# Kernel tuning notes

Measured on AMD Instinct MI355X. Metric: run time of the kernel, lower is better.

## Reference

```python
import jax, jax.numpy as jnp
import numpy as np

# ---- static problem constants ----
B, N, L = 8, 256, 15.0          # molecules, atoms per molecule, cubic cell length (Angstrom)
DL, SIGMA = 1.5, 1.0            # Ewald k-space spacing and Gaussian smearing width
ELEMENTS = np.array([1, 6, 7, 8])
NORM_FACTOR = (1.0 / 90.0474) ** 0.5
TWO_PI = 2.0 * np.pi
KSQ_MAX = (TWO_PI / DL) ** 2
NMAX = int(np.ceil(L / DL))     # 10 -> (2*10+1)^3 = 9261 k-vectors
_g = np.arange(-NMAX, NMAX + 1)
K_GRID = jnp.asarray(np.stack(np.meshgrid(_g, _g, _g, indexing='ij'), -1)
                     .reshape(-1, 3).astype(np.float32))  # [K,3] integer k indices
_zmap = np.full(int(ELEMENTS.max()) + 1, -1)
for _i, _z in enumerate(ELEMENTS):
    _zmap[_z] = _i
Z_INDEX_MAP = jnp.asarray(_zmap)


def setup_inputs() -> dict:
    key = jax.random.key(0)
    k1, k2, k3, k4 = jax.random.split(key, 4)
    positions = jax.random.uniform(k1, (B * N, 3), jnp.float32) * L
    cell = jnp.tile((L * jnp.eye(3, dtype=jnp.float32))[None], (B, 1, 1))
    chi = jax.random.normal(k2, (B * N,), jnp.float32)
    idx = jax.random.randint(k3, (B * N,), 0, len(ELEMENTS))
    atomic_numbers = jnp.asarray(ELEMENTS)[idx]
    batch = jnp.repeat(jnp.arange(B), N)
    J_raw = jax.random.uniform(k4, (len(ELEMENTS),), jnp.float32, 0.5, 1.5)
    system_charge = jnp.zeros((B,), jnp.float32)
    return dict(positions=positions, cell=cell, chi=chi, J_raw=J_raw,
                system_charge=system_charge, atomic_numbers=atomic_numbers, batch=batch)


def _a_matrix(r, cell):
    """Reciprocal-space Ewald interaction matrix A (energy = 0.5 q^T A q), one molecule."""
    recip = TWO_PI * jnp.linalg.inv(cell).T            # rows: reciprocal lattice vectors
    k = K_GRID @ recip                                 # [K,3]
    k2 = jnp.sum(k * k, axis=-1)                       # [K]
    valid = (k2 > 1e-10) & (k2 < KSQ_MAX)
    f = jnp.where(valid, jnp.exp(-0.5 * SIGMA * SIGMA * k2) / jnp.maximum(k2, 1e-10), 0.0)
    vol = jnp.abs(jnp.linalg.det(cell))
    kr = r @ k.T                                       # [N,K]
    c, s = jnp.cos(kr), jnp.sin(kr)
    # A_ij = (4*pi/V) sum_k f(k) cos(k.(r_i - r_j))
    A = (2.0 * TWO_PI / vol) * ((c * f) @ c.T + (s * f) @ s.T)
    # remove Gaussian self-interaction: E_self = -sum_i q_i^2 / (sigma*sqrt(2*pi))
    A = A - (2.0 / (SIGMA * np.sqrt(TWO_PI))) * jnp.eye(N, dtype=r.dtype)
    return A


def _solve_qeq(A, chi_m, J_i, Q):
    """Charge-equilibration with Lagrange multiplier for total-charge constraint."""
    coeffs = jnp.ones((N + 1, N + 1), A.dtype)
    coeffs = coeffs.at[:N, :N].set(A + jnp.diag(J_i))
    coeffs = coeffs.at[N, N].set(0.0)
    rhs = jnp.concatenate([-chi_m, (Q / NORM_FACTOR)[None].astype(A.dtype)])
    sol = jnp.linalg.solve(coeffs, rhs)
    q = sol[:N]
    e = 0.5 * q @ (A @ q)
    return q, e


def reference(positions, cell, chi, J_raw, system_charge, atomic_numbers, batch):
    r = positions.reshape(B, N, 3)
    chi_b = chi.reshape(B, N)
    J_elem = jnp.square(J_raw)
    J_i = J_elem[Z_INDEX_MAP[atomic_numbers]].reshape(B, N)
    A = jax.vmap(_a_matrix)(r, cell)                   # [B,N,N]
    q, e = jax.vmap(_solve_qeq)(A, chi_b, J_i, system_charge)
    all_q_eq = q.reshape(B * N, 1)
    all_ewald = e                                      # [B]
    return all_q_eq, all_ewald
```

## Files before the change

### kernel.cpp

```cpp
#include <hip/hip_runtime.h>
#include <math.h>

#define NBATCH 8
#define NATOM  256
#define NP1    257
#define WROW   258
#define TOTALK 9261
#define KCAP   2560
#define KC     16
#define NB     16
#define UBW    124
#define BDF    768
#define BDB    256
#define FLAGOFF 2528
#define SLOTMAX 2500

#define TWO_PI_D 6.283185307179586
#define DIAG_SUB 0.7978845608028654

__device__ __constant__ int TI10[10] = {0,0,0,0,1,1,1,2,2,3};
__device__ __constant__ int TJ10[10] = {0,1,2,3,1,2,3,2,3,3};

struct GemmSh {
  int4   kn[KC];
  double kw[KC];
  double cI[KC][64], sI[KC][64];
  double cJ[KC][64], sJ[KC][64];
};

__device__ __forceinline__ void atomAddD(double* p, double v) {
#if defined(__has_builtin)
#if __has_builtin(__builtin_amdgcn_global_atomic_fadd_f64)
  __builtin_amdgcn_global_atomic_fadd_f64(p, v);
  return;
#endif
#endif
  unsigned long long* u = (unsigned long long*)p;
  unsigned long long old = *u, assumed;
  do {
    assumed = old;
    old = atomicCAS(u, assumed,
                    (unsigned long long)__double_as_longlong(
                        v + __longlong_as_double((long long)assumed)));
  } while (old != assumed);
}

__device__ __forceinline__ void classify2(const void* c0, const void* c1, const void* c2,
                                          const float*& chi, const int*& znum)
{
  const void* cands[3] = {c0, c1, c2};
  int got = 0;
  for (int i = 0; i < 3; i++) {
    unsigned uu = ((const unsigned*)cands[i])[0];
    if (uu == 0u) continue;
    else if (uu < 16u) { znum = (const int*)cands[i]; got |= 1; }
    else               { chi  = (const float*)cands[i]; got |= 2; }
  }
  if (got != 3) { chi = (const float*)c0; znum = (const int*)c1; }
}

__global__ __launch_bounds__(256) void zero_planes(
    double* __restrict__ P0g, int4* __restrict__ klist, int nplanes)
{
  if (blockIdx.x == 0 && threadIdx.x < 256) {
    const int b = threadIdx.x >> 5, s = threadIdx.x & 31;
    klist[(size_t)b*KCAP + FLAGOFF + s] = make_int4(0, 0, 0, 0);
  }
  const size_t npair = (size_t)nplanes * NBATCH * ((NP1*WROW) >> 1);
  double2* Z = (double2*)P0g;
  const double2 z = make_double2(0.0, 0.0);
  for (size_t i = (size_t)blockIdx.x*256 + threadIdx.x; i < npair;
       i += (size_t)gridDim.x*256)
    Z[i] = z;
}

__global__ __launch_bounds__(256) void prep(
    const float* __restrict__ pos, const float* __restrict__ cell,
    double2* __restrict__ Tg, int4* __restrict__ klist,
    double* __restrict__ kw, int* __restrict__ kcount,
    const void* __restrict__ c0, const void* __restrict__ c1, const void* __restrict__ c2,
    const float* __restrict__ syschg,
    double* __restrict__ P0g, int nplanes)
{
  const int b = blockIdx.x;
  const int tid = threadIdx.x;
  __shared__ double ivs[9];
  __shared__ double prefs;
  __shared__ int cnt;
  if (tid == 0) {
    double c[9];
#pragma unroll
    for (int i = 0; i < 9; i++) c[i] = (double)cell[b*9+i];
    double det = c[0]*(c[4]*c[8]-c[5]*c[7]) - c[1]*(c[3]*c[8]-c[5]*c[6])
               + c[2]*(c[3]*c[7]-c[4]*c[6]);
    double idet = 1.0/det;
    ivs[0]=(c[4]*c[8]-c[5]*c[7])*idet; ivs[1]=(c[2]*c[7]-c[1]*c[8])*idet; ivs[2]=(c[1]*c[5]-c[2]*c[4])*idet;
    ivs[3]=(c[5]*c[6]-c[3]*c[8])*idet; ivs[4]=(c[0]*c[8]-c[2]*c[6])*idet; ivs[5]=(c[2]*c[3]-c[0]*c[5])*idet;
    ivs[6]=(c[3]*c[7]-c[4]*c[6])*idet; ivs[7]=(c[1]*c[6]-c[0]*c[7])*idet; ivs[8]=(c[0]*c[4]-c[1]*c[3])*idet;
    prefs = 2.0*TWO_PI_D/fabs(det);
    cnt = 0;
  }
  __syncthreads();
  {
    const int a = tid;
    double x = (double)pos[((size_t)b*NATOM+a)*3+0];
    double y = (double)pos[((size_t)b*NATOM+a)*3+1];
    double z = (double)pos[((size_t)b*NATOM+a)*3+2];
    double u[3];
    u[0] = TWO_PI_D*(ivs[0]*x + ivs[3]*y + ivs[6]*z);
    u[1] = TWO_PI_D*(ivs[1]*x + ivs[4]*y + ivs[7]*z);
    u[2] = TWO_PI_D*(ivs[2]*x + ivs[5]*y + ivs[8]*z);
#pragma unroll
    for (int d = 0; d < 3; d++) {
      double2* T = Tg + (size_t)((b*3 + d)*21)*256;
      double c1 = cos(u[d]);
      double s1 = sin(u[d]);
      T[10*256 + a] = make_double2(1.0, 0.0);
      T[11*256 + a] = make_double2(c1,  s1);
      T[ 9*256 + a] = make_double2(c1, -s1);
      double cp = c1, sp = s1;
      for (int n = 2; n <= 10; n++) {
        double cn = cp*c1 - sp*s1;
        double sn = sp*c1 + cp*s1;
        cp = cn; sp = sn;
        T[(10+n)*256 + a] = make_double2(cp,  sp);
        T[(10-n)*256 + a] = make_double2(cp, -sp);
      }
    }
  }
  const double ksqmax = (TWO_PI_D/1.5)*(TWO_PI_D/1.5);
  for (int m = tid; m < TOTALK; m += 256) {
    int n1 = m/441 - 10;
    int n2 = (m/21)%21 - 10;
    int n3 = m%21 - 10;
    bool half = (n1 > 0) || (n1 == 0 && (n2 > 0 || (n2 == 0 && n3 > 0)));
    if (!half) continue;
    double d1 = n1, d2 = n2, d3 = n3;
    double kx = TWO_PI_D*(ivs[0]*d1 + ivs[1]*d2 + ivs[2]*d3);
    double ky = TWO_PI_D*(ivs[3]*d1 + ivs[4]*d2 + ivs[5]*d3);
    double kz = TWO_PI_D*(ivs[6]*d1 + ivs[7]*d2 + ivs[8]*d3);
    double k2 = kx*kx + ky*ky + kz*kz;
    if (k2 > 1e-10 && k2 < ksqmax) {
      double w = 2.0 * prefs * exp(-0.5*k2) / k2;
      int slot = atomicAdd(&cnt, 1);
      if (slot < SLOTMAX) {
        klist[b*KCAP + slot] = make_int4(n1, n2, n3, 0);
        kw[b*KCAP + slot] = w;
      }
    }
  }
  __syncthreads();
  {
    const float* chi = nullptr; const int* znum = nullptr;
    classify2(c0, c1, c2, chi, znum);
    double* P0b = P0g + (size_t)b*NP1*WROW;
    for (int i = tid; i < NATOM; i += 256) {
      P0b[(size_t)NATOM*WROW + i] = 1.0;
      P0b[(size_t)i*WROW + NATOM] = 1.0;
      P0b[(size_t)i*WROW + 257]   = -(double)chi[b*NATOM + i];
    }
    if (tid == 0) {
      P0b[(size_t)NATOM*WROW + NATOM] = 0.0;
      P0b[(size_t)NATOM*WROW + 257]   = (double)syschg[b]*sqrt(90.0474);
      kcount[b] = (cnt < SLOTMAX) ? cnt : SLOTMAX;
    }
  }
}

__device__ void gemm_tile(int b, int ti, int tj, int tid,
                          const double2* __restrict__ Tg,
                          const int4* __restrict__ klist,
                          const double* __restrict__ kw, int ks, int ke,
                          double* __restrict__ Ab, bool mirror, GemmSh& S)
{
  const int tx = tid & 15, ty = tid >> 4;
  const int ro = ty << 2, co = tx << 2;
  double acc[16];
#pragma unroll
  for (int i = 0; i < 16; i++) acc[i] = 0.0;

  for (int k0 = ks; k0 < ke; k0 += KC) {
    if (tid < KC) {
      int kk = k0 + tid;
      if (kk < ke) { S.kn[tid] = klist[b*KCAP + kk]; S.kw[tid] = kw[b*KCAP + kk]; }
      else         { S.kn[tid] = make_int4(0,0,0,0); S.kw[tid] = 0.0; }
    }
    __syncthreads();
#pragma unroll
    for (int p = 0; p < 8; p++) {
      int idx = p*256 + tid;
      int a    = idx & 63;
      int kk   = (idx >> 6) & (KC-1);
      int side = idx >> 10;
      int atom = ((side == 0) ? ti : tj) + a;
      int4 nn = S.kn[kk];
      double2 t1 = Tg[(size_t)((b*3+0)*21 + (nn.x+10))*256 + atom];
      double2 t2 = Tg[(size_t)((b*3+1)*21 + (nn.y+10))*256 + atom];
      double2 t3 = Tg[(size_t)((b*3+2)*21 + (nn.z+10))*256 + atom];
      double ex = t1.x*t2.x - t1.y*t2.y;
      double ey = t1.x*t2.y + t1.y*t2.x;
      double cx = ex*t3.x - ey*t3.y;
      double cy = ex*t3.y + ey*t3.x;
      if (side == 0) { double w = S.kw[kk]; S.cI[kk][a] = w*cx; S.sI[kk][a] = w*cy; }
      else           { S.cJ[kk][a] = cx; S.sJ[kk][a] = cy; }
    }
    __syncthreads();
#pragma unroll
    for (int kk = 0; kk < KC; kk++) {
      double ci[4], si[4], cj[4], sj[4];
#pragma unroll
      for (int r = 0; r < 2; r++) {
        double2 v0 = *(const double2*)&S.cI[kk][ro + 2*r];
        ci[2*r] = v0.x; ci[2*r+1] = v0.y;
        double2 v1 = *(const double2*)&S.sI[kk][ro + 2*r];
        si[2*r] = v1.x; si[2*r+1] = v1.y;
        double2 v2 = *(const double2*)&S.cJ[kk][co + 2*r];
        cj[2*r] = v2.x; cj[2*r+1] = v2.y;
        double2 v3 = *(const double2*)&S.sJ[kk][co + 2*r];
        sj[2*r] = v3.x; sj[2*r+1] = v3.y;
      }
#pragma unroll
      for (int r = 0; r < 4; r++)
#pragma unroll
        for (int c = 0; c < 4; c++)
          acc[r*4+c] += ci[r]*cj[c] + si[r]*sj[c];
    }
    __syncthreads();
  }
#pragma unroll
  for (int r = 0; r < 4; r++) {
#pragma unroll
    for (int c = 0; c < 4; c++) {
      int gr = ti + ro + r, gc = tj + co + c;
      double v = acc[r*4+c];
      atomAddD(&Ab[(size_t)gr*WROW + gc], v);
      if (mirror && ti != tj) atomAddD(&Ab[(size_t)gc*WROW + gr], v);
    }
  }
}

__device__ __forceinline__ double* plane_sel(double* P0, double* P1, double* P2, int s) {
  return (s == 0) ? P0 : ((s == 1) ? P1 : P2);
}

__global__ __launch_bounds__(256) void build_A_gemm(
    const double2* __restrict__ Tg, const int4* __restrict__ klist,
    const double* __restrict__ kw, const int* __restrict__ kcount,
    double* __restrict__ P0g, double* __restrict__ P1g, double* __restrict__ P2g,
    int nplanes)
{
  __shared__ GemmSh S;
  const int nseg = 2*nplanes;
  const int u = blockIdx.x;
  const int seg = u / 80;
  const int r = u - seg*80;
  const int b = r / 10;
  const int t = r - b*10;
  const int s = (seg < nplanes) ? seg : (seg - nplanes);
  const int cnt = kcount[b];
  const int ks = (int)((long long)cnt * seg / nseg);
  const int ke = (int)((long long)cnt * (seg+1) / nseg);
  double* Ab = plane_sel(P0g, P1g, P2g, s) + (size_t)b*NP1*WROW;
  gemm_tile(b, TI10[t]*64, TJ10[t]*64, threadIdx.x, Tg, klist, kw, ks, ke, Ab, true, S);
}

__global__ __launch_bounds__(BDF, 2) void solve_factor(
    double* __restrict__ P0g, const double* __restrict__ P1g, const double* __restrict__ P2g,
    int nplanes,
    const void* __restrict__ c0, const void* __restrict__ c1, const void* __restrict__ c2,
    const float* __restrict__ Jraw,
    int4* __restrict__ klist, double* __restrict__ U11g)
{
  const int b = blockIdx.x >> 1;
  const int h = blockIdx.x & 1;
  const int tid = threadIdx.x;
  double* Pb = P0g + (size_t)b*NP1*WROW;
  const double* Qb = P1g + (size_t)b*NP1*WROW;
  const double* Rb = P2g + (size_t)b*NP1*WROW;
  const bool two   = (nplanes > 1);
  const bool three = (nplanes > 2);
  int* FA = (int*)(klist + (size_t)b*KCAP + FLAGOFF);
  int* FB = FA + 32;
  double* U11b = U11g + (size_t)b*17*256;

  __shared__ __align__(16) double pan[NP1+4][NB+2];
  __shared__ double dnv[NB];
  __shared__ __align__(16) double Ub[NB][UBW];

  const float* chi = nullptr; const int* znum = nullptr;
  classify2(c0, c1, c2, chi, znum);
  const float J0 = Jraw[0], J1 = Jraw[1], J2 = Jraw[2], J3 = Jraw[3];

  int p = 0;
  for (int p0 = 0; p0 < NP1; p0 += NB, p++) {
    const int pw  = (NB < NP1 - p0) ? NB : (NP1 - p0);
    const int nr  = NP1 - p0;
    const int nrt = nr - pw;
    const int tc0 = p0 + pw;
    const int tc  = WROW - tc0;
    const bool first = (p0 == 0);
    int leftCols = (tc >= 4) ? (((tc >> 1) + 1) & ~1) : tc;
    const int clo = (h == 0) ? tc0 : tc0 + leftCols;
    const int chiC = (h == 0) ? tc0 + leftCols : tc0 + tc;
    const int ownCols = chiC - clo;
    if (p > 0) {
      if (tid == 0) {
        while (atomicAdd(&FA[p-1], 0) == 0) __builtin_amdgcn_s_sleep(2);
        while (atomicAdd(&FB[p-1], 0) == 0) __builtin_amdgcn_s_sleep(2);
        __threadfence();
      }
      __syncthreads();
    }
    for (int idx = tid; idx < nr*pw; idx += BDF) {
      int r, c;
      if (pw == NB) { r = idx >> 4; c = idx & 15; } else { r = idx; c = 0; }
      double v;
      if (first) {
        size_t a = (size_t)r*WROW + c;
        v = Pb[a];
        if (two)   v += Qb[a];
        if (three) v += Rb[a];
        if (r == c) {
          int z = znum[b*NATOM + r];
          float Jr = (z == 1) ? J0 : (z == 6) ? J1 : (z == 7) ? J2 : J3;
          v += (double)Jr*(double)Jr - DIAG_SUB;
        }
      } else {
        v = Pb[(size_t)(p0+r)*WROW + p0 + c];
      }
      pan[r][c] = v;
    }
    __syncthreads();
    if (pw == NB) {
      if (tid < NB) {
        double v[NB];
#pragma unroll
        for (int c = 0; c < NB; c++) v[c] = pan[tid][c];
#pragma unroll
        for (int c = 0; c < NB; c++) {
          double piv = __shfl(v[c], c);
          double dinv = 1.0 / piv;
          if (tid == c) dnv[c] = dinv;
          double f = v[c] * dinv;
#pragma unroll
          for (int cc = 0; cc < NB; cc++) {
            if (cc > c) {
              double ucc = __shfl(v[cc], c);
              if (tid > c) v[cc] -= f * ucc;
            }
          }
          if (tid > c) v[c] = f;
        }
#pragma unroll
        for (int c = 0; c < NB; c++) pan[tid][c] = v[c];
      }
    }
    __syncthreads();
    if (pw == NB) {
      if (tid < nrt) {
        const int r = NB + tid;
        double w[NB];
#pragma unroll
        for (int c = 0; c < NB; c++) w[c] = pan[r][c];
#pragma unroll
        for (int c = 0; c < NB; c++) {
          double s = w[c];
#pragma unroll
          for (int c2 = 0; c2 < NB; c2++) if (c2 < c) s -= w[c2] * pan[c2][c];
          w[c] = s * dnv[c];
        }
#pragma unroll
        for (int c = 0; c < NB; c++) pan[r][c] = w[c];
      } else if (tid >= 256 && tid < 256 + ownCols) {
        const int j = clo + (tid - 256);
        double v[NB];
#pragma unroll
        for (int c = 0; c < NB; c++) {
          size_t a = (size_t)(p0+c)*WROW + j;
          double t = Pb[a];
          if (first) {
            if (two)   t += Qb[a];
            if (three) t += Rb[a];
          }
          v[c] = t;
        }
#pragma unroll
        for (int c = 0; c < NB; c++)
#pragma unroll
          for (int r2 = 0; r2 < NB; r2++) if (r2 > c) v[r2] -= pan[r2][c]*v[c];
#pragma unroll
        for (int c = 0; c < NB; c++) {
          Pb[(size_t)(p0+c)*WROW + j] = v[c];
          Ub[c][tid - 256] = v[c];
        }
      } else if (h == 0 && tid >= 512) {
        const int idx = tid - 512;
        U11b[p*256 + idx] = pan[idx >> 4][idx & 15];
      }
    } else {
      if (h == 0 && tid == 0) U11b[16*256] = pan[0][0];
    }
    __syncthreads();
    if (pw == NB && ownCols > 0 && nrt > 0) {
      const int jp   = tid & 63;
      const int rowg = tid >> 6;
      if (clo + 2*jp < chiC) {
        const int jrel = (clo - tc0) + 2*jp;
        double va[NB], vb[NB];
#pragma unroll
        for (int c = 0; c < NB; c++) {
          double2 u = *(const double2*)&Ub[c][2*jp];
          va[c] = u.x; vb[c] = u.y;
        }
        auto loadrow = [&](int rr, double2& x0, double2& x1) {
          x0 = make_double2(0.0, 0.0); x1 = x0;
          if (rr < nrt) {
            const int row0 = tc0 + rr;
            const size_t ad = (size_t)row0*WROW + tc0 + jrel;
            x0 = *(const double2*)&Pb[ad];
            if (rr + 1 < nrt) x1 = *(const double2*)&Pb[ad + WROW];
            if (first) {
              if (two) {
                double2 q0 = *(const double2*)&Qb[ad]; x0.x += q0.x; x0.y += q0.y;
                if (rr + 1 < nrt) { double2 q1 = *(const double2*)&Qb[ad + WROW]; x1.x += q1.x; x1.y += q1.y; }
              }
              if (three) {
                double2 r0v = *(const double2*)&Rb[ad]; x0.x += r0v.x; x0.y += r0v.y;
                if (rr + 1 < nrt) { double2 r1v = *(const double2*)&Rb[ad + WROW]; x1.x += r1v.x; x1.y += r1v.y; }
              }
              if (rr == jrel) {
                const int row0g = tc0 + rr;
                if (row0g < NATOM) {
                  int z = znum[b*NATOM + row0g];
                  float Jr = (z == 1) ? J0 : (z == 6) ? J1 : (z == 7) ? J2 : J3;
                  x0.x += (double)Jr*(double)Jr - DIAG_SUB;
                }
                if (rr + 1 < nrt && row0g + 1 < NATOM) {
                  int z = znum[b*NATOM + row0g + 1];
                  float Jr = (z == 1) ? J0 : (z == 6) ? J1 : (z == 7) ? J2 : J3;
                  x1.y += (double)Jr*(double)Jr - DIAG_SUB;
                }
              }
            }
          }
        };
        int rr = 2*rowg;
        double2 a0, a1;
        loadrow(rr, a0, a1);
        while (rr < nrt) {
          const int rn = rr + 24;
          double2 n0, n1;
          loadrow(rn, n0, n1);
          const double* pr0 = pan[NB + rr];
          const double* pr1 = pan[NB + rr + 1];
#pragma unroll
          for (int m = 0; m < NB/2; m++) {
            double2 l0 = *(const double2*)&pr0[2*m];
            double2 l1 = *(const double2*)&pr1[2*m];
            a0.x -= l0.x*va[2*m] + l0.y*va[2*m+1];
            a0.y -= l0.x*vb[2*m] + l0.y*vb[2*m+1];
            a1.x -= l1.x*va[2*m] + l1.y*va[2*m+1];
            a1.y -= l1.x*vb[2*m] + l1.y*vb[2*m+1];
          }
          const size_t ad = (size_t)(tc0+rr)*WROW + tc0 + jrel;
          *(double2*)&Pb[ad] = a0;
          if (rr + 1 < nrt) *(double2*)&Pb[ad + WROW] = a1;
          a0 = n0; a1 = n1;
          rr = rn;
        }
      }
    }
    __syncthreads();
    if (pw == NB && tid == 0) {
      __threadfence();
      if (h == 0) atomicExch(&FA[p], 1);
      else        atomicExch(&FB[p], 1);
    }
  }
}

__global__ __launch_bounds__(BDB) void solve_back(
    double* __restrict__ P0g, const double* __restrict__ U11g,
    const void* __restrict__ c0, const void* __restrict__ c1, const void* __restrict__ c2,
    const float* __restrict__ Jraw, const float* __restrict__ syschg,
    float* __restrict__ out)
{
  const int b = blockIdx.x;
  const int tid = threadIdx.x;
  double* Pb = P0g + (size_t)b*NP1*WROW;
  const double* U11b = U11g + (size_t)b*17*256;

  __shared__ double panb[NB][NB+1];
  __shared__ double xs[NP1];
  __shared__ double red[BDB];

  const float* chi = nullptr; const int* znum = nullptr;
  classify2(c0, c1, c2, chi, znum);
  const double rhsN = (double)syschg[b] * sqrt(90.0474);
  const float J0 = Jraw[0], J1 = Jraw[1], J2 = Jraw[2], J3 = Jraw[3];

  for (int r = tid; r < NP1; r += BDB) xs[r] = Pb[(size_t)r*WROW + 257];
  __syncthreads();
  for (int pb0 = 256; pb0 >= 0; pb0 -= NB) {
    const int w = (pb0 == 256) ? 1 : NB;
    if (w == NB) {
      {
        const int i = tid >> 4, c = tid & 15;
        panb[i][c] = U11b[(pb0 >> 4)*256 + i*16 + c];
      }
      __syncthreads();
      if (tid < NB) {
        double u[NB];
#pragma unroll
        for (int c = 0; c < NB; c++) u[c] = panb[tid][c];
        double y  = xs[pb0 + tid];
        double di = 1.0 / panb[tid][tid];
        double xr = 0.0;
#pragma unroll
        for (int i = NB-1; i >= 0; i--) {
          double xi = y * di;
          xi = __shfl(xi, i);
          if (tid == i) xr = xi;
          if (tid < i)  y -= u[i] * xi;
        }
        xs[pb0 + tid] = xr;
      }
    } else {
      if (tid == 0) xs[256] = xs[256] / U11b[16*256];
    }
    __syncthreads();
    if (tid < pb0) {
      const double* rowp = &Pb[(size_t)tid*WROW + pb0];
      double s = 0.0;
      for (int c = 0; c < w; c++) s += rowp[c]*xs[pb0+c];
      xs[tid] -= s;
    }
    __syncthreads();
  }

  out[b*NATOM + tid] = (float)xs[tid];
  const double lam = xs[NATOM];
  double q  = xs[tid];
  double ch = (double)chi[b*NATOM + tid];
  int z = znum[b*NATOM + tid];
  float Jr = (z == 1) ? J0 : (z == 6) ? J1 : (z == 7) ? J2 : J3;
  red[tid] = q*ch + (double)Jr*(double)Jr*q*q;
  __syncthreads();
  for (int st = BDB/2; st > 0; st >>= 1) {
    if (tid < st) red[tid] += red[tid + st];
    __syncthreads();
  }
  if (tid == 0)
    out[NBATCH*NATOM + b] = (float)(-0.5*(red[0] + lam*rhsN));
}

extern "C" void kernel_launch(void* const* d_in, const int* in_sizes, int n_in,
                              void* d_out, int out_size, void* d_ws, size_t ws_size,
                              hipStream_t stream)
{
  int iPos=-1, iCell=-1, iJ=-1, iQ=-1, cand[3]={-1,-1,-1}, nc=0;
  for (int i = 0; i < n_in; i++) {
    int s = in_sizes[i];
    if      (s == 6144) iPos  = i;
    else if (s == 72)   iCell = i;
    else if (s == 4)    iJ    = i;
    else if (s == 8)    iQ    = i;
    else if (s == 2048 && nc < 3) cand[nc++] = i;
  }
  if (!(iPos>=0 && iCell>=0 && iJ>=0 && iQ>=0 && nc>=2)) {
    iPos=iCell=iJ=iQ=-1; nc=0; cand[0]=cand[1]=cand[2]=-1;
    for (int i = 0; i < n_in; i++) {
      int s = in_sizes[i];
      if      (s == 24576) iPos  = i;
      else if (s == 288)   iCell = i;
      else if (s == 16)    iJ    = i;
      else if (s == 32)    iQ    = i;
      else if (s == 8192 && nc < 3) cand[nc++] = i;
    }
  }
  if (!(iPos>=0 && iCell>=0 && iJ>=0 && iQ>=0 && nc>=2)) {
    iPos=0; iCell=1; iJ=3; iQ=4; cand[0]=2; cand[1]=5; cand[2]=6; nc=3;
  }
  if (nc == 2) cand[2] = cand[1];

  const float* pos  = (const float*)d_in[iPos];
  const float* cell = (const float*)d_in[iCell];
  const float* Jraw = (const float*)d_in[iJ];
  const float* sysq = (const float*)d_in[iQ];
  const void*  c0   = d_in[cand[0]];
  const void*  c1   = d_in[cand[1]];
  const void*  c2   = d_in[cand[2]];
  float* out = (float*)d_out;

  const size_t planeB = (size_t)NBATCH*NP1*WROW*sizeof(double);
  const size_t tgB = 2064384, klB = 327680, kwB = 163840;
  const size_t trigAll = tgB + klB + kwB + 64;
  int nplanes = (ws_size >= 3*planeB + trigAll) ? 3 :
                ((ws_size >= 2*planeB + trigAll) ? 2 : 1);

  char* ws = (char*)d_ws;
  double*  P0g = (double*)ws;
  double*  P1g = (nplanes > 1) ? (double*)(ws + planeB)   : P0g;
  double*  P2g = (nplanes > 2) ? (double*)(ws + 2*planeB) : P1g;
  char* trigBase = ws + (size_t)nplanes*planeB;
  double2* Tg     = (double2*)trigBase;
  int4*    klist  = (int4*)  (trigBase + tgB);
  double*  kwa    = (double*)(trigBase + tgB + klB);
  int*     kcount = (int*)   (trigBase + tgB + klB + kwB);
  double*  U11g   = (double*)trigBase;

  hipLaunchKernelGGL(zero_planes,  dim3(512),           dim3(256), 0, stream,
                     P0g, klist, nplanes);
  hipLaunchKernelGGL(prep,         dim3(NBATCH),        dim3(256), 0, stream,
                     pos, cell, Tg, klist, kwa, kcount, c0, c1, c2, sysq,
                     P0g, nplanes);
  hipLaunchKernelGGL(build_A_gemm, dim3(160*nplanes),   dim3(256), 0, stream,
                     Tg, klist, kwa, kcount, P0g, P1g, P2g, nplanes);
  hipLaunchKernelGGL(solve_factor, dim3(2*NBATCH),      dim3(BDF), 0, stream,
                     P0g, P1g, P2g, nplanes, c0, c1, c2, Jraw, klist, U11g);
  hipLaunchKernelGGL(solve_back,   dim3(NBATCH),        dim3(BDB), 0, stream,
                     P0g, U11g, c0, c1, c2, Jraw, sysq, out);
}
```

Before: 591.1 us.

## Replace atomic accumulation with per-segment planes and a merge kernel

When the workspace is large enough, the A-matrix GEMM now writes each k-segment's partial sums into its own plane with plain stores instead of double atomics. This removes the need to zero the planes beforehand. A new merge kernel then adds planes 3-5 into planes 0-2, and the factor kernel still sums three planes. The aim is to drop the atomic read-modify-write traffic and the zeroing pass. The cost is an extra kernel launch, more workspace, and a merge pass over three planes of memory.

```diff
diff --git a/kernel.cpp b/kernel.cpp
--- a/kernel.cpp
+++ b/kernel.cpp
@@ -60,13 +60,14 @@
 }
 
 __global__ __launch_bounds__(256) void zero_planes(
-    double* __restrict__ P0g, int4* __restrict__ klist, int nplanes)
+    double* __restrict__ P0g, int4* __restrict__ klist, int nzero)
 {
   if (blockIdx.x == 0 && threadIdx.x < 256) {
     const int b = threadIdx.x >> 5, s = threadIdx.x & 31;
     klist[(size_t)b*KCAP + FLAGOFF + s] = make_int4(0, 0, 0, 0);
   }
-  const size_t npair = (size_t)nplanes * NBATCH * ((NP1*WROW) >> 1);
+  if (nzero <= 0) return;
+  const size_t npair = (size_t)nzero * NBATCH * ((NP1*WROW) >> 1);
   double2* Z = (double2*)P0g;
   const double2 z = make_double2(0.0, 0.0);
   for (size_t i = (size_t)blockIdx.x*256 + threadIdx.x; i < npair;
@@ -80,7 +81,8 @@
     double* __restrict__ kw, int* __restrict__ kcount,
     const void* __restrict__ c0, const void* __restrict__ c1, const void* __restrict__ c2,
     const float* __restrict__ syschg,
-    double* __restrict__ P0g, int nplanes)
+    double* __restrict__ P0g, double* __restrict__ P1g, double* __restrict__ P2g,
+    int nplanes)
 {
   const int b = blockIdx.x;
   const int tid = threadIdx.x;
@@ -154,14 +156,34 @@
     const float* chi = nullptr; const int* znum = nullptr;
     classify2(c0, c1, c2, chi, znum);
     double* P0b = P0g + (size_t)b*NP1*WROW;
+    double* P1b = P1g + (size_t)b*NP1*WROW;
+    double* P2b = P2g + (size_t)b*NP1*WROW;
     for (int i = tid; i < NATOM; i += 256) {
       P0b[(size_t)NATOM*WROW + i] = 1.0;
       P0b[(size_t)i*WROW + NATOM] = 1.0;
       P0b[(size_t)i*WROW + 257]   = -(double)chi[b*NATOM + i];
+      if (nplanes > 1) {
+        P1b[(size_t)NATOM*WROW + i] = 0.0;
+        P1b[(size_t)i*WROW + NATOM] = 0.0;
+        P1b[(size_t)i*WROW + 257]   = 0.0;
+      }
+      if (nplanes > 2) {
+        P2b[(size_t)NATOM*WROW + i] = 0.0;
+        P2b[(size_t)i*WROW + NATOM] = 0.0;
+        P2b[(size_t)i*WROW + 257]   = 0.0;
+      }
     }
     if (tid == 0) {
       P0b[(size_t)NATOM*WROW + NATOM] = 0.0;
       P0b[(size_t)NATOM*WROW + 257]   = (double)syschg[b]*sqrt(90.0474);
+      if (nplanes > 1) {
+        P1b[(size_t)NATOM*WROW + NATOM] = 0.0;
+        P1b[(size_t)NATOM*WROW + 257]   = 0.0;
+      }
+      if (nplanes > 2) {
+        P2b[(size_t)NATOM*WROW + NATOM] = 0.0;
+        P2b[(size_t)NATOM*WROW + 257]   = 0.0;
+      }
       kcount[b] = (cnt < SLOTMAX) ? cnt : SLOTMAX;
     }
   }
@@ -171,7 +193,8 @@
                           const double2* __restrict__ Tg,
                           const int4* __restrict__ klist,
                           const double* __restrict__ kw, int ks, int ke,
-                          double* __restrict__ Ab, bool mirror, GemmSh& S)
+                          double* __restrict__ Ab, bool mirror, bool useAtomic,
+                          GemmSh& S)
 {
   const int tx = tid & 15, ty = tid >> 4;
   const int ro = ty << 2, co = tx << 2;
@@ -233,35 +256,67 @@
     for (int c = 0; c < 4; c++) {
       int gr = ti + ro + r, gc = tj + co + c;
       double v = acc[r*4+c];
-      atomAddD(&Ab[(size_t)gr*WROW + gc], v);
-      if (mirror && ti != tj) atomAddD(&Ab[(size_t)gc*WROW + gr], v);
-    }
-  }
-}
-
-__device__ __forceinline__ double* plane_sel(double* P0, double* P1, double* P2, int s) {
-  return (s == 0) ? P0 : ((s == 1) ? P1 : P2);
+      if (useAtomic) {
+        atomAddD(&Ab[(size_t)gr*WROW + gc], v);
+        if (mirror && ti != tj) atomAddD(&Ab[(size_t)gc*WROW + gr], v);
+      } else {
+        Ab[(size_t)gr*WROW + gc] = v;
+        if (mirror && ti != tj) Ab[(size_t)gc*WROW + gr] = v;
+      }
+    }
+  }
 }
 
 __global__ __launch_bounds__(256) void build_A_gemm(
     const double2* __restrict__ Tg, const int4* __restrict__ klist,
     const double* __restrict__ kw, const int* __restrict__ kcount,
     double* __restrict__ P0g, double* __restrict__ P1g, double* __restrict__ P2g,
-    int nplanes)
+    double* __restrict__ P3g, double* __restrict__ P4g, double* __restrict__ P5g,
+    int nplanes, int accMode)
 {
   __shared__ GemmSh S;
-  const int nseg = 2*nplanes;
+  const int nseg = (accMode == 0) ? 6 : 2*nplanes;
   const int u = blockIdx.x;
   const int seg = u / 80;
   const int r = u - seg*80;
   const int b = r / 10;
   const int t = r - b*10;
-  const int s = (seg < nplanes) ? seg : (seg - nplanes);
+  int s;
+  double* base;
+  if (accMode == 0) {
+    s = seg;
+    base = (s == 0) ? P0g : (s == 1) ? P1g : (s == 2) ? P2g
+         : (s == 3) ? P3g : (s == 4) ? P4g : P5g;
+  } else {
+    s = (seg < nplanes) ? seg : (seg - nplanes);
+    base = (s == 0) ? P0g : (s == 1) ? P1g : P2g;
+  }
   const int cnt = kcount[b];
   const int ks = (int)((long long)cnt * seg / nseg);
   const int ke = (int)((long long)cnt * (seg+1) / nseg);
-  double* Ab = plane_sel(P0g, P1g, P2g, s) + (size_t)b*NP1*WROW;
-  gemm_tile(b, TI10[t]*64, TJ10[t]*64, threadIdx.x, Tg, klist, kw, ks, ke, Ab, true, S);
+  double* Ab = base + (size_t)b*NP1*WROW;
+  gemm_tile(b, TI10[t]*64, TJ10[t]*64, threadIdx.x, Tg, klist, kw, ks, ke, Ab,
+            true, accMode != 0, S);
+}
+
+__global__ __launch_bounds__(256) void merge_planes(double* __restrict__ P0g)
+{
+  const size_t per = (size_t)NP1*WROW >> 1;
+  double2* B = (double2*)P0g;
+  const size_t nwork = (size_t)3*NBATCH*256*128;
+  for (size_t i = (size_t)blockIdx.x*256 + threadIdx.x; i < nwork;
+       i += (size_t)gridDim.x*256) {
+    const int c2 = (int)(i & 127);
+    size_t t = i >> 7;
+    const int rr = (int)(t & 255);
+    const int pb = (int)(t >> 8);
+    const size_t d = (size_t)pb*per + (size_t)rr*129 + c2;
+    const size_t sidx = d + 24*per;
+    double2 a = B[d];
+    const double2 x = B[sidx];
+    a.x += x.x; a.y += x.y;
+    B[d] = a;
+  }
 }
 
 __global__ __launch_bounds__(BDF, 2) void solve_factor(
@@ -595,29 +650,42 @@
   const size_t planeB = (size_t)NBATCH*NP1*WROW*sizeof(double);
   const size_t tgB = 2064384, klB = 327680, kwB = 163840;
   const size_t trigAll = tgB + klB + kwB + 64;
-  int nplanes = (ws_size >= 3*planeB + trigAll) ? 3 :
-                ((ws_size >= 2*planeB + trigAll) ? 2 : 1);
+  int nacc;
+  if      (ws_size >= 6*planeB + trigAll) nacc = 6;
+  else if (ws_size >= 3*planeB + trigAll) nacc = 3;
+  else if (ws_size >= 2*planeB + trigAll) nacc = 2;
+  else                                    nacc = 1;
+  const int nplanes = (nacc >= 3) ? 3 : nacc;
+  const int accMode = (nacc == 6) ? 0 : 1;
 
   char* ws = (char*)d_ws;
   double*  P0g = (double*)ws;
-  double*  P1g = (nplanes > 1) ? (double*)(ws + planeB)   : P0g;
-  double*  P2g = (nplanes > 2) ? (double*)(ws + 2*planeB) : P1g;
-  char* trigBase = ws + (size_t)nplanes*planeB;
+  double*  P1g = (nacc > 1) ? (double*)(ws + planeB)   : P0g;
+  double*  P2g = (nacc > 2) ? (double*)(ws + 2*planeB) : P1g;
+  double*  P3g = (nacc > 3) ? (double*)(ws + 3*planeB) : P0g;
+  double*  P4g = (nacc > 4) ? (double*)(ws + 4*planeB) : P0g;
+  double*  P5g = (nacc > 5) ? (double*)(ws + 5*planeB) : P0g;
+  char* trigBase = ws + (size_t)nacc*planeB;
   double2* Tg     = (double2*)trigBase;
   int4*    klist  = (int4*)  (trigBase + tgB);
   double*  kwa    = (double*)(trigBase + tgB + klB);
   int*     kcount = (int*)   (trigBase + tgB + klB + kwB);
   double*  U11g   = (double*)trigBase;
 
-  hipLaunchKernelGGL(zero_planes,  dim3(512),           dim3(256), 0, stream,
-                     P0g, klist, nplanes);
-  hipLaunchKernelGGL(prep,         dim3(NBATCH),        dim3(256), 0, stream,
+  const int nseg = (accMode == 0) ? 6 : 2*nplanes;
+
+  hipLaunchKernelGGL(zero_planes,  dim3(512),       dim3(256), 0, stream,
+                     P0g, klist, (accMode == 1) ? nplanes : 0);
+  hipLaunchKernelGGL(prep,         dim3(NBATCH),    dim3(256), 0, stream,
                      pos, cell, Tg, klist, kwa, kcount, c0, c1, c2, sysq,
-                     P0g, nplanes);
-  hipLaunchKernelGGL(build_A_gemm, dim3(160*nplanes),   dim3(256), 0, stream,
-                     Tg, klist, kwa, kcount, P0g, P1g, P2g, nplanes);
-  hipLaunchKernelGGL(solve_factor, dim3(2*NBATCH),      dim3(BDF), 0, stream,
+                     P0g, P1g, P2g, nplanes);
+  hipLaunchKernelGGL(build_A_gemm, dim3(80*nseg),   dim3(256), 0, stream,
+                     Tg, klist, kwa, kcount, P0g, P1g, P2g, P3g, P4g, P5g,
+                     nplanes, accMode);
+  if (accMode == 0)
+    hipLaunchKernelGGL(merge_planes, dim3(512),     dim3(256), 0, stream, P0g);
+  hipLaunchKernelGGL(solve_factor, dim3(2*NBATCH),  dim3(BDF), 0, stream,
                      P0g, P1g, P2g, nplanes, c0, c1, c2, Jraw, klist, U11g);
-  hipLaunchKernelGGL(solve_back,   dim3(NBATCH),        dim3(BDB), 0, stream,
+  hipLaunchKernelGGL(solve_back,   dim3(NBATCH),    dim3(BDB), 0, stream,
                      P0g, U11g, c0, c1, c2, Jraw, sysq, out);
 }
```

Result: faster. 542.3 us (-8.2%).
